# Kernel tuning notes

Hardware: AMD Instinct MI355X
Metric: run time of the kernel (lower is better)

The kernel has to match this reference:

```python
import jax, jax.numpy as jnp
import numpy as np

N_NODES = 100000

def _sage_conv(x, src, dst, deg_inv, Wl, bl, Wr):
    # PyG SAGEConv (aggr='mean', root_weight=True):
    #   out = lin_l(mean_{j in N(i)} x_j) + lin_r(x_i)
    msg = x[src]                                            # [E, d]
    agg = jax.ops.segment_sum(msg, dst, num_segments=N_NODES)  # [N, d]
    agg = agg * deg_inv                                     # mean (0 for isolated nodes)
    return agg @ Wl.T + bl + x @ Wr.T


def setup_inputs() -> dict:
    key = jax.random.key(0)
    ks = jax.random.split(key, 12)
    N, E, d_in, d_h, d_out = N_NODES, 1600000, 64, 64, 32
    x = jax.random.normal(ks[0], (N, d_in), dtype=jnp.float32)
    edge_index = jax.random.randint(ks[1], (2, E), 0, N, dtype=jnp.int64)

    def glorot(k, shape):
        fan_in = shape[1]
        return jax.random.normal(k, shape, dtype=jnp.float32) / np.sqrt(fan_in)

    return {
        "x": x,
        "edge_index": edge_index,
        "W1l": glorot(ks[2], (d_h, d_in)), "b1l": jnp.zeros((d_h,), jnp.float32), "W1r": glorot(ks[3], (d_h, d_in)),
        "W2l": glorot(ks[4], (d_h, d_h)),  "b2l": jnp.zeros((d_h,), jnp.float32), "W2r": glorot(ks[5], (d_h, d_h)),
        "W3l": glorot(ks[6], (d_h, d_h)),  "b3l": jnp.zeros((d_h,), jnp.float32), "W3r": glorot(ks[7], (d_h, d_h)),
        "Wfc": glorot(ks[8], (d_out, d_h)), "bfc": jnp.zeros((d_out,), jnp.float32),
    }


def reference(x, edge_index, W1l, b1l, W1r, W2l, b2l, W2r, W3l, b3l, W3r, Wfc, bfc):
    src, dst = edge_index[0], edge_index[1]
    # in-degree per destination node (shared by all three conv layers)
    ones = jnp.ones((src.shape[0],), x.dtype)
    deg = jax.ops.segment_sum(ones, dst, num_segments=N_NODES)
    deg_inv = (1.0 / jnp.maximum(deg, 1.0))[:, None]        # [N, 1]

    h = jax.nn.relu(_sage_conv(x, src, dst, deg_inv, W1l, b1l, W1r))
    # dropout(p=0.5) is identity in eval mode
    h = jax.nn.relu(_sage_conv(h, src, dst, deg_inv, W2l, b2l, W2r))
    h = jax.nn.relu(_sage_conv(h, src, dst, deg_inv, W3l, b3l, W3r))
    return h @ Wfc.T + bfc
```

## Files before the change

### kernel.cpp

```cpp
#include <hip/hip_runtime.h>
#include <hip/hip_fp16.h>

#define N_NODES 100000
#define D 64
#define BR 256
#define NB 391
#define ECH 4096
#define NROWPAD 100096

typedef _Float16 f16x8 __attribute__((ext_vector_type(8)));
typedef float f32x4 __attribute__((ext_vector_type(4)));

__device__ __forceinline__ float rlf(float v, int l) {
    union { float f; int i; } u;
    u.f = v;
    u.i = __builtin_amdgcn_readlane(u.i, l);
    return u.f;
}

__global__ __launch_bounds__(256) void k_cvt(const float4* __restrict__ x,
                                             uint2* __restrict__ y, int n4) {
    int i = blockIdx.x * 256 + threadIdx.x;
    if (i < n4) {
        float4 v = x[i];
        union { __half2 h[2]; uint2 u; } pk;
        pk.h[0] = __floats2half2_rn(v.x, v.y);
        pk.h[1] = __floats2half2_rn(v.z, v.w);
        y[i] = pk.u;
    }
}

__global__ __launch_bounds__(256) void k_prep(const float* __restrict__ Wl1, const float* __restrict__ Wr1,
                                              const float* __restrict__ Wl2, const float* __restrict__ Wr2,
                                              const float* __restrict__ Wl3, const float* __restrict__ Wr3,
                                              const float* __restrict__ Wfc,
                                              __half* __restrict__ Wf1, __half* __restrict__ Wf2,
                                              __half* __restrict__ Wf3, __half* __restrict__ Wffc,
                                              unsigned* __restrict__ x16, unsigned* __restrict__ H1,
                                              unsigned* __restrict__ H2) {
    int t = blockIdx.x * 256 + threadIdx.x;
    if (t < 24576) {
        int layer = t / 8192;
        int r = t % 8192;
        int f = r >> 9, rem = r & 511;
        int lane = rem >> 3, i = rem & 7;
        int kt = f >> 2, nt = f & 3;
        int k = kt * 32 + (lane >> 4) * 8 + i;
        int o = nt * 16 + (lane & 15);
        const float* Wl = layer == 0 ? Wl1 : layer == 1 ? Wl2 : Wl3;
        const float* Wr = layer == 0 ? Wr1 : layer == 1 ? Wr2 : Wr3;
        float v = (k < 64) ? Wl[o * 64 + k] : Wr[o * 64 + (k - 64)];
        __half* Wf = layer == 0 ? Wf1 : layer == 1 ? Wf2 : Wf3;
        Wf[r] = __float2half(v);
    } else if (t < 26624) {
        int r = t - 24576;
        int f = r >> 9, rem = r & 511;
        int lane = rem >> 3, i = rem & 7;
        int kt = f >> 1, nt = f & 1;
        int k = kt * 32 + (lane >> 4) * 8 + i;
        int o = nt * 16 + (lane & 15);
        Wffc[r] = __float2half(Wfc[o * 64 + k]);
    } else if (t < 26720) {
        int z = t - 26624;
        unsigned* buf = (z >> 5) == 0 ? x16 : (z >> 5) == 1 ? H1 : H2;
        buf[(size_t)N_NODES * 32 + (z & 31)] = 0u;
    }
}


__global__ __launch_bounds__(256) void k_hist(const int* __restrict__ dst,
                                              int* __restrict__ histT,
                                              int E, int ga) {
    __shared__ int h[NB];
    int blk = blockIdx.x, tid = threadIdx.x;
    for (int i = tid; i < NB; i += 256) h[i] = 0;
    __syncthreads();
    int base = blk * ECH;
    int lim = E - base; if (lim > ECH) lim = ECH;
    for (int i = tid; i < lim; i += 256)
        atomicAdd(&h[dst[base + i] >> 8], 1);
    __syncthreads();
    for (int i = tid; i < NB; i += 256)
        histT[i * ga + blk] = h[i];
}

__global__ __launch_bounds__(256) void k_scan1(const int* __restrict__ cnt,
                                               int* __restrict__ part,
                                               int* __restrict__ bsums) {
    __shared__ int s[256];
    int tid = threadIdx.x;
    int i4 = blockIdx.x * 256 + tid;
    int4 v = reinterpret_cast<const int4*>(cnt)[i4];
    int tsum = v.x + v.y + v.z + v.w;
    s[tid] = tsum;
    __syncthreads();
    for (int off = 1; off < 256; off <<= 1) {
        int t = 0;
        if (tid >= off) t = s[tid - off];
        __syncthreads();
        if (tid >= off) s[tid] += t;
        __syncthreads();
    }
    int excl = tid ? s[tid - 1] : 0;
    if (tid == 255) bsums[blockIdx.x] = s[255];
    int4 o;
    o.x = excl;
    o.y = o.x + v.x;
    o.z = o.y + v.y;
    o.w = o.z + v.z;
    reinterpret_cast<int4*>(part)[i4] = o;
}

__global__ __launch_bounds__(256) void k_scan2(int* __restrict__ bsums, int nb,
                                               int* __restrict__ col) {
    __shared__ int s[256];
    int tid = threadIdx.x;
    if (tid < 8) col[tid] = N_NODES;
    int v = (tid < nb) ? bsums[tid] : 0;
    s[tid] = v;
    __syncthreads();
    for (int off = 1; off < 256; off <<= 1) {
        int t = 0;
        if (tid >= off) t = s[tid - off];
        __syncthreads();
        if (tid >= off) s[tid] += t;
        __syncthreads();
    }
    if (tid < nb) bsums[tid] = tid ? s[tid - 1] : 0;
}

__global__ __launch_bounds__(256) void k_part(const int* __restrict__ src,
                                              const int* __restrict__ dst,
                                              const int* __restrict__ offs,
                                              const int* __restrict__ bsums,
                                              int* __restrict__ bedge,
                                              int E, int ga) {
    __shared__ int o[NB];
    int blk = blockIdx.x, tid = threadIdx.x;
    for (int i = tid; i < NB; i += 256) {
        int ent = i * ga + blk;
        o[i] = offs[ent] + bsums[ent >> 10];
    }
    __syncthreads();
    int base = blk * ECH;
    int lim = E - base; if (lim > ECH) lim = ECH;
    for (int i = tid; i < lim; i += 256) {
        int e = base + i;
        int d = dst[e];
        int pos = atomicAdd(&o[d >> 8], 1);
        bedge[pos] = src[e] | ((d & 255) << 17);
    }
}

__global__ __launch_bounds__(256) void k_csr(const int* __restrict__ bedge,
                                             const int* __restrict__ offs,
                                             const int* __restrict__ bsums,
                                             int* __restrict__ col,
                                             int2* __restrict__ rp,
                                             float* __restrict__ deg_inv,
                                             int E, int ga) {
    __shared__ int lcnt[BR];
    __shared__ int stmp[BR];
    __shared__ int lcur[BR];
    int b = blockIdx.x, tid = threadIdx.x;
    int e0 = b * ga;
    int ebeg = offs[e0] + bsums[e0 >> 10];
    int eend = E;
    if (b + 1 < NB) {
        int e1 = (b + 1) * ga;
        eend = offs[e1] + bsums[e1 >> 10];
    }
    int nbase = b * BR;
    int cbase = ebeg + b * (BR * 4) + 8;
    lcnt[tid] = 0;
    __syncthreads();
    for (int e = ebeg + tid; e < eend; e += 256)
        atomicAdd(&lcnt[bedge[e] >> 17], 1);
    __syncthreads();
    int v = lcnt[tid];
    int pdeg = (v + 3) & ~3;
    stmp[tid] = pdeg;
    __syncthreads();
    for (int off = 1; off < 256; off <<= 1) {
        int t = 0;
        if (tid >= off) t = stmp[tid - off];
        __syncthreads();
        if (tid >= off) stmp[tid] += t;
        __syncthreads();
    }
    int ex = tid ? stmp[tid - 1] : 0;
    int slot = cbase + ex;
    lcur[tid] = slot;
    int node = nbase + tid;
    if (node < N_NODES) {
        rp[node] = make_int2(slot, slot + pdeg);
        deg_inv[node] = 1.0f / (float)(v > 1 ? v : 1);
        for (int s2 = slot + v; s2 < slot + pdeg; ++s2) col[s2] = N_NODES;
    }
    __syncthreads();
    for (int e = ebeg + tid; e < eend; e += 256) {
        int ed = bedge[e];
        int pos = atomicAdd(&lcur[ed >> 17], 1);
        col[pos] = ed & 0x1FFFF;
    }
}


__global__ __launch_bounds__(256) void k_fused(const __half* __restrict__ Hin,
                                               __half* __restrict__ Hout,
                                               const __half* __restrict__ Wf,
                                               const float* __restrict__ bias,
                                               const int2* __restrict__ rp,
                                               const int* __restrict__ col,
                                               const float* __restrict__ deg_inv, int n) {
    __shared__ __half lds[4][16][72];
    int l = threadIdx.x & 63;
    int wv = threadIdx.x >> 6;
    int m0 = blockIdx.x * 64 + wv * 16;
    int q = l >> 4, li = l & 15;

    int beg = 0, nq = 0;
    float dinv = 0.f;
    if (l < 16 && m0 + l < n) {
        int2 se = rp[m0 + l];
        beg = se.x;
        nq = (se.y - se.x) >> 2;
        dinv = deg_inv[m0 + l];
    }
    const uint2* x8 = (const uint2*)Hin;
    const int* cq = col + q;

#pragma unroll
    for (int g = 0; g < 4; ++g) {
        int b0 = __builtin_amdgcn_readlane(beg, 4 * g + 0);
        int b1 = __builtin_amdgcn_readlane(beg, 4 * g + 1);
        int b2 = __builtin_amdgcn_readlane(beg, 4 * g + 2);
        int b3 = __builtin_amdgcn_readlane(beg, 4 * g + 3);
        int c0 = __builtin_amdgcn_readlane(nq, 4 * g + 0);
        int c1 = __builtin_amdgcn_readlane(nq, 4 * g + 1);
        int c2 = __builtin_amdgcn_readlane(nq, 4 * g + 2);
        int c3 = __builtin_amdgcn_readlane(nq, 4 * g + 3);
        int qmax = max(max(c0, c1), max(c2, c3));
        __half2 s00 = __floats2half2_rn(0.f, 0.f), s01 = s00;
        __half2 s10 = s00, s11 = s00, s20 = s00, s21 = s00, s30 = s00, s31 = s00;
        for (int qq = 0; qq < qmax; qq += 2) {
            int o = qq * 4;
            int a0 = qq < c0 ? b0 + o : 0;
            int a1 = qq < c1 ? b1 + o : 0;
            int a2 = qq < c2 ? b2 + o : 0;
            int a3 = qq < c3 ? b3 + o : 0;
            int a4 = qq + 1 < c0 ? b0 + o + 4 : 0;
            int a5 = qq + 1 < c1 ? b1 + o + 4 : 0;
            int a6 = qq + 1 < c2 ? b2 + o + 4 : 0;
            int a7 = qq + 1 < c3 ? b3 + o + 4 : 0;
            int i0 = cq[a0], i1 = cq[a1], i2 = cq[a2], i3 = cq[a3];
            int i4 = cq[a4], i5 = cq[a5], i6 = cq[a6], i7 = cq[a7];
            uint2 u0 = x8[(size_t)i0 * 16 + li];
            uint2 u1 = x8[(size_t)i1 * 16 + li];
            uint2 u2 = x8[(size_t)i2 * 16 + li];
            uint2 u3 = x8[(size_t)i3 * 16 + li];
            uint2 u4 = x8[(size_t)i4 * 16 + li];
            uint2 u5 = x8[(size_t)i5 * 16 + li];
            uint2 u6 = x8[(size_t)i6 * 16 + li];
            uint2 u7 = x8[(size_t)i7 * 16 + li];
            union { unsigned v; __half2 h; } w;
            w.v = u0.x; s00 = __hadd2(s00, w.h);
            w.v = u0.y; s01 = __hadd2(s01, w.h);
            w.v = u1.x; s10 = __hadd2(s10, w.h);
            w.v = u1.y; s11 = __hadd2(s11, w.h);
            w.v = u2.x; s20 = __hadd2(s20, w.h);
            w.v = u2.y; s21 = __hadd2(s21, w.h);
            w.v = u3.x; s30 = __hadd2(s30, w.h);
            w.v = u3.y; s31 = __hadd2(s31, w.h);
            w.v = u4.x; s00 = __hadd2(s00, w.h);
            w.v = u4.y; s01 = __hadd2(s01, w.h);
            w.v = u5.x; s10 = __hadd2(s10, w.h);
            w.v = u5.y; s11 = __hadd2(s11, w.h);
            w.v = u6.x; s20 = __hadd2(s20, w.h);
            w.v = u6.y; s21 = __hadd2(s21, w.h);
            w.v = u7.x; s30 = __hadd2(s30, w.h);
            w.v = u7.y; s31 = __hadd2(s31, w.h);
        }
        union { __half2 h; int i; } t;
#pragma unroll
        for (int m = 16; m < 64; m <<= 1) {
            t.h = s00; t.i = __shfl_xor(t.i, m); s00 = __hadd2(s00, t.h);
            t.h = s01; t.i = __shfl_xor(t.i, m); s01 = __hadd2(s01, t.h);
            t.h = s10; t.i = __shfl_xor(t.i, m); s10 = __hadd2(s10, t.h);
            t.h = s11; t.i = __shfl_xor(t.i, m); s11 = __hadd2(s11, t.h);
            t.h = s20; t.i = __shfl_xor(t.i, m); s20 = __hadd2(s20, t.h);
            t.h = s21; t.i = __shfl_xor(t.i, m); s21 = __hadd2(s21, t.h);
            t.h = s30; t.i = __shfl_xor(t.i, m); s30 = __hadd2(s30, t.h);
            t.h = s31; t.i = __shfl_xor(t.i, m); s31 = __hadd2(s31, t.h);
        }
        float d0 = rlf(dinv, 4 * g + 0);
        float d1 = rlf(dinv, 4 * g + 1);
        float d2 = rlf(dinv, 4 * g + 2);
        float d3 = rlf(dinv, 4 * g + 3);
        if (l < 16) {
            union { __half2 h; unsigned v; } p0, p1;
            float2 f;
            uint2 ov;
            f = __half22float2(s00); p0.h = __floats2half2_rn(f.x * d0, f.y * d0);
            f = __half22float2(s01); p1.h = __floats2half2_rn(f.x * d0, f.y * d0);
            ov.x = p0.v; ov.y = p1.v;
            *(uint2*)&lds[wv][4 * g + 0][li * 4] = ov;
            f = __half22float2(s10); p0.h = __floats2half2_rn(f.x * d1, f.y * d1);
            f = __half22float2(s11); p1.h = __floats2half2_rn(f.x * d1, f.y * d1);
            ov.x = p0.v; ov.y = p1.v;
            *(uint2*)&lds[wv][4 * g + 1][li * 4] = ov;
            f = __half22float2(s20); p0.h = __floats2half2_rn(f.x * d2, f.y * d2);
            f = __half22float2(s21); p1.h = __floats2half2_rn(f.x * d2, f.y * d2);
            ov.x = p0.v; ov.y = p1.v;
            *(uint2*)&lds[wv][4 * g + 2][li * 4] = ov;
            f = __half22float2(s30); p0.h = __floats2half2_rn(f.x * d3, f.y * d3);
            f = __half22float2(s31); p1.h = __floats2half2_rn(f.x * d3, f.y * d3);
            ov.x = p0.v; ov.y = p1.v;
            *(uint2*)&lds[wv][4 * g + 3][li * 4] = ov;
        }
    }

    const f16x8* wf8 = (const f16x8*)Wf;
    f16x8 bf[4][4];
#pragma unroll
    for (int kt = 0; kt < 4; ++kt)
#pragma unroll
        for (int nt = 0; nt < 4; ++nt)
            bf[kt][nt] = wf8[(kt * 4 + nt) * 64 + l];
    int rowA = li;
    f32x4 acc[4];
#pragma unroll
    for (int nt = 0; nt < 4; ++nt) {
        float bs = bias[nt * 16 + rowA];
        acc[nt] = (f32x4){bs, bs, bs, bs};
    }
#pragma unroll
    for (int kt = 0; kt < 4; ++kt) {
        f16x8 a;
        if (kt < 2)
            a = *(const f16x8*)&lds[wv][rowA][kt * 32 + q * 8];
        else
            a = *(const f16x8*)(Hin + (size_t)(m0 + rowA) * D + (kt - 2) * 32 + q * 8);
#pragma unroll
        for (int nt = 0; nt < 4; ++nt)
            acc[nt] = __builtin_amdgcn_mfma_f32_16x16x32_f16(a, bf[kt][nt], acc[nt], 0, 0, 0);
    }
#pragma unroll
    for (int nt = 0; nt < 4; ++nt)
#pragma unroll
        for (int qd = 0; qd < 4; ++qd) {
            int node = m0 + q * 4 + qd;
            float v = fmaxf(acc[nt][qd], 0.f);
            if (node < n)
                Hout[(size_t)node * D + nt * 16 + rowA] = __float2half(v);
        }
}


template <int KT, int NT, bool RELU, bool TWO, bool HOUT>
__global__ __launch_bounds__(256) void k_mgemm(const __half* __restrict__ A,
                                               const __half* __restrict__ X,
                                               const __half* __restrict__ Wf,
                                               const float* __restrict__ bias,
                                               void* __restrict__ outp, int n) {
    int l = threadIdx.x & 63;
    int wv = threadIdx.x >> 6;
    int m0 = blockIdx.x * 64 + wv * 16;
    int rowA = l & 15;
    int kg = l >> 4;
    const f16x8* wf8 = (const f16x8*)Wf;
    f16x8 b[KT][NT];
#pragma unroll
    for (int kt = 0; kt < KT; ++kt)
#pragma unroll
        for (int nt = 0; nt < NT; ++nt)
            b[kt][nt] = wf8[(kt * NT + nt) * 64 + l];
    f32x4 acc[NT];
#pragma unroll
    for (int nt = 0; nt < NT; ++nt) {
        float bs = bias[nt * 16 + rowA];
        acc[nt] = (f32x4){bs, bs, bs, bs};
    }
#pragma unroll
    for (int kt = 0; kt < KT; ++kt) {
        const __half* sp = (TWO && kt >= KT / 2) ? X : A;
        int ko = (TWO ? (kt & (KT / 2 - 1)) : kt) * 32;
        f16x8 a = *(const f16x8*)(sp + (size_t)(m0 + rowA) * D + ko + kg * 8);
#pragma unroll
        for (int nt = 0; nt < NT; ++nt)
            acc[nt] = __builtin_amdgcn_mfma_f32_16x16x32_f16(a, b[kt][nt], acc[nt], 0, 0, 0);
    }
#pragma unroll
    for (int nt = 0; nt < NT; ++nt)
#pragma unroll
        for (int q = 0; q < 4; ++q) {
            int node = m0 + kg * 4 + q;
            float v = acc[nt][q];
            if (RELU) v = fmaxf(v, 0.f);
            if (node < n) {
                if (HOUT)
                    ((__half*)outp)[(size_t)node * D + nt * 16 + rowA] = __float2half(v);
                else
                    ((float*)outp)[(size_t)node * (NT * 16) + nt * 16 + rowA] = v;
            }
        }
}


extern "C" void kernel_launch(void* const* d_in, const int* in_sizes, int n_in,
                              void* d_out, int out_size, void* d_ws, size_t ws_size,
                              hipStream_t stream) {
    const float* x   = (const float*)d_in[0];
    const int*   ei  = (const int*)d_in[1];
    const int    E   = in_sizes[1] / 2;
    const int*   src = ei;
    const int*   dst = ei + E;
    const float* W1l = (const float*)d_in[2];
    const float* b1l = (const float*)d_in[3];
    const float* W1r = (const float*)d_in[4];
    const float* W2l = (const float*)d_in[5];
    const float* b2l = (const float*)d_in[6];
    const float* W2r = (const float*)d_in[7];
    const float* W3l = (const float*)d_in[8];
    const float* b3l = (const float*)d_in[9];
    const float* W3r = (const float*)d_in[10];
    const float* Wfc = (const float*)d_in[11];
    const float* bfc = (const float*)d_in[12];
    float* out = (float*)d_out;

    const int ga      = (E + ECH - 1) / ECH;
    const int entries = NB * ga;
    const int padded  = (entries + 1023) & ~1023;
    const int nb2     = padded / 1024;

    char* p = (char*)d_ws;
    size_t off = 0;
    auto take = [&](size_t bytes) -> void* {
        void* r = p + off;
        off = (off + bytes + 255) & ~(size_t)255;
        return r;
    };
    __half* x16    = (__half*)take((size_t)NROWPAD * D * 2);
    __half* H1     = (__half*)take((size_t)NROWPAD * D * 2);
    __half* H2     = (__half*)take((size_t)NROWPAD * D * 2);
    float* deg_inv = (float*)take((size_t)N_NODES * 4);
    int2*  rp      = (int2*)take((size_t)N_NODES * 8);
    int*   histT   = (int*)take((size_t)padded * 4);
    int*   offs    = (int*)take((size_t)padded * 4);
    int*   bsums   = (int*)take(256 * 4);
    int*   bedge   = (int*)take((size_t)E * 4);
    int*   col     = (int*)take((size_t)(E + NB * BR * 4 + 72) * 4);
    __half* Wf1    = (__half*)take(8192 * 2);
    __half* Wf2    = (__half*)take(8192 * 2);
    __half* Wf3    = (__half*)take(8192 * 2);
    __half* Wffc   = (__half*)take(2048 * 2);

    k_prep<<<105, 256, 0, stream>>>(W1l, W1r, W2l, W2r, W3l, W3r, Wfc,
                                    Wf1, Wf2, Wf3, Wffc,
                                    (unsigned*)x16, (unsigned*)H1, (unsigned*)H2);
    int n4 = N_NODES * D / 4;
    k_cvt<<<(n4 + 255) / 256, 256, 0, stream>>>((const float4*)x, (uint2*)x16, n4);

    hipMemsetAsync(histT, 0, (size_t)padded * 4, stream);
    k_hist<<<ga, 256, 0, stream>>>(dst, histT, E, ga);
    k_scan1<<<nb2, 256, 0, stream>>>(histT, offs, bsums);
    k_scan2<<<1, 256, 0, stream>>>(bsums, nb2, col);
    k_part<<<ga, 256, 0, stream>>>(src, dst, offs, bsums, bedge, E, ga);
    k_csr<<<NB, 256, 0, stream>>>(bedge, offs, bsums, col, rp, deg_inv, E, ga);

    int gg = NROWPAD / 64;

    k_fused<<<gg, 256, 0, stream>>>(x16, H1, Wf1, b1l, rp, col, deg_inv, N_NODES);
    k_fused<<<gg, 256, 0, stream>>>(H1, H2, Wf2, b2l, rp, col, deg_inv, N_NODES);
    k_fused<<<gg, 256, 0, stream>>>(H2, H1, Wf3, b3l, rp, col, deg_inv, N_NODES);
    k_mgemm<2, 2, false, false, false><<<gg, 256, 0, stream>>>(H1, nullptr, Wffc, bfc, out, N_NODES);
}
```

Measured before the change: 187.4 us.

## Fuse final FC into third SAGE layer, fold memset into prep, retune partition

The final linear layer now runs inside the third fused SAGE kernel: the ReLU'd layer-3 tile is staged in LDS and multiplied by the FC weights. This removes a full write and re-read of H1 and one kernel launch. The histogram memset moves into the prep kernel, and the histogram and partition kernels use 512-thread blocks over smaller edge chunks for more parallelism. The trade-offs are more per-block histogram columns to scan and more LDS and register pressure in the last kernel.

```diff
diff --git a/kernel.cpp b/kernel.cpp
--- a/kernel.cpp
+++ b/kernel.cpp
@@ -5,7 +5,7 @@
 #define D 64
 #define BR 256
 #define NB 391
-#define ECH 4096
+#define ECH 2560
 #define NROWPAD 100096
 
 typedef _Float16 f16x8 __attribute__((ext_vector_type(8)));
@@ -37,7 +37,8 @@
                                               __half* __restrict__ Wf1, __half* __restrict__ Wf2,
                                               __half* __restrict__ Wf3, __half* __restrict__ Wffc,
                                               unsigned* __restrict__ x16, unsigned* __restrict__ H1,
-                                              unsigned* __restrict__ H2) {
+                                              unsigned* __restrict__ H2,
+                                              int* __restrict__ histT, int padded) {
     int t = blockIdx.x * 256 + threadIdx.x;
     if (t < 24576) {
         int layer = t / 8192;
@@ -64,23 +65,25 @@
         int z = t - 26624;
         unsigned* buf = (z >> 5) == 0 ? x16 : (z >> 5) == 1 ? H1 : H2;
         buf[(size_t)N_NODES * 32 + (z & 31)] = 0u;
-    }
-}
-
-
-__global__ __launch_bounds__(256) void k_hist(const int* __restrict__ dst,
+    } else if (t >= 32768 && t < 32768 + padded) {
+        histT[t - 32768] = 0;
+    }
+}
+
+
+__global__ __launch_bounds__(512) void k_hist(const int* __restrict__ dst,
                                               int* __restrict__ histT,
                                               int E, int ga) {
     __shared__ int h[NB];
     int blk = blockIdx.x, tid = threadIdx.x;
-    for (int i = tid; i < NB; i += 256) h[i] = 0;
+    for (int i = tid; i < NB; i += 512) h[i] = 0;
     __syncthreads();
     int base = blk * ECH;
     int lim = E - base; if (lim > ECH) lim = ECH;
-    for (int i = tid; i < lim; i += 256)
+    for (int i = tid; i < lim; i += 512)
         atomicAdd(&h[dst[base + i] >> 8], 1);
     __syncthreads();
-    for (int i = tid; i < NB; i += 256)
+    for (int i = tid; i < NB; i += 512)
         histT[i * ga + blk] = h[i];
 }
 
@@ -129,7 +132,7 @@
     if (tid < nb) bsums[tid] = tid ? s[tid - 1] : 0;
 }
 
-__global__ __launch_bounds__(256) void k_part(const int* __restrict__ src,
+__global__ __launch_bounds__(512) void k_part(const int* __restrict__ src,
                                               const int* __restrict__ dst,
                                               const int* __restrict__ offs,
                                               const int* __restrict__ bsums,
@@ -137,14 +140,14 @@
                                               int E, int ga) {
     __shared__ int o[NB];
     int blk = blockIdx.x, tid = threadIdx.x;
-    for (int i = tid; i < NB; i += 256) {
+    for (int i = tid; i < NB; i += 512) {
         int ent = i * ga + blk;
         o[i] = offs[ent] + bsums[ent >> 10];
     }
     __syncthreads();
     int base = blk * ECH;
     int lim = E - base; if (lim > ECH) lim = ECH;
-    for (int i = tid; i < lim; i += 256) {
+    for (int i = tid; i < lim; i += 512) {
         int e = base + i;
         int d = dst[e];
         int pos = atomicAdd(&o[d >> 8], 1);
@@ -206,19 +209,15 @@
 }
 
 
-__global__ __launch_bounds__(256) void k_fused(const __half* __restrict__ Hin,
-                                               __half* __restrict__ Hout,
-                                               const __half* __restrict__ Wf,
-                                               const float* __restrict__ bias,
-                                               const int2* __restrict__ rp,
-                                               const int* __restrict__ col,
-                                               const float* __restrict__ deg_inv, int n) {
-    __shared__ __half lds[4][16][72];
-    int l = threadIdx.x & 63;
-    int wv = threadIdx.x >> 6;
-    int m0 = blockIdx.x * 64 + wv * 16;
+__device__ __forceinline__ void fused_core(const __half* __restrict__ Hin,
+                                           const __half* __restrict__ Wf,
+                                           const float* __restrict__ bias,
+                                           const int2* __restrict__ rp,
+                                           const int* __restrict__ col,
+                                           const float* __restrict__ deg_inv, int n,
+                                           __half (&lds)[16][72], int m0, int l,
+                                           f32x4 (&acc)[4]) {
     int q = l >> 4, li = l & 15;
-
     int beg = 0, nq = 0;
     float dinv = 0.f;
     if (l < 16 && m0 + l < n) {
@@ -304,19 +303,19 @@
             f = __half22float2(s00); p0.h = __floats2half2_rn(f.x * d0, f.y * d0);
             f = __half22float2(s01); p1.h = __floats2half2_rn(f.x * d0, f.y * d0);
             ov.x = p0.v; ov.y = p1.v;
-            *(uint2*)&lds[wv][4 * g + 0][li * 4] = ov;
+            *(uint2*)&lds[4 * g + 0][li * 4] = ov;
             f = __half22float2(s10); p0.h = __floats2half2_rn(f.x * d1, f.y * d1);
             f = __half22float2(s11); p1.h = __floats2half2_rn(f.x * d1, f.y * d1);
             ov.x = p0.v; ov.y = p1.v;
-            *(uint2*)&lds[wv][4 * g + 1][li * 4] = ov;
+            *(uint2*)&lds[4 * g + 1][li * 4] = ov;
             f = __half22float2(s20); p0.h = __floats2half2_rn(f.x * d2, f.y * d2);
             f = __half22float2(s21); p1.h = __floats2half2_rn(f.x * d2, f.y * d2);
             ov.x = p0.v; ov.y = p1.v;
-            *(uint2*)&lds[wv][4 * g + 2][li * 4] = ov;
+            *(uint2*)&lds[4 * g + 2][li * 4] = ov;
             f = __half22float2(s30); p0.h = __floats2half2_rn(f.x * d3, f.y * d3);
             f = __half22float2(s31); p1.h = __floats2half2_rn(f.x * d3, f.y * d3);
             ov.x = p0.v; ov.y = p1.v;
-            *(uint2*)&lds[wv][4 * g + 3][li * 4] = ov;
+            *(uint2*)&lds[4 * g + 3][li * 4] = ov;
         }
     }
 
@@ -328,7 +327,6 @@
         for (int nt = 0; nt < 4; ++nt)
             bf[kt][nt] = wf8[(kt * 4 + nt) * 64 + l];
     int rowA = li;
-    f32x4 acc[4];
 #pragma unroll
     for (int nt = 0; nt < 4; ++nt) {
         float bs = bias[nt * 16 + rowA];
@@ -338,13 +336,29 @@
     for (int kt = 0; kt < 4; ++kt) {
         f16x8 a;
         if (kt < 2)
-            a = *(const f16x8*)&lds[wv][rowA][kt * 32 + q * 8];
+            a = *(const f16x8*)&lds[rowA][kt * 32 + q * 8];
         else
             a = *(const f16x8*)(Hin + (size_t)(m0 + rowA) * D + (kt - 2) * 32 + q * 8);
 #pragma unroll
         for (int nt = 0; nt < 4; ++nt)
             acc[nt] = __builtin_amdgcn_mfma_f32_16x16x32_f16(a, bf[kt][nt], acc[nt], 0, 0, 0);
     }
+}
+
+__global__ __launch_bounds__(256) void k_fused(const __half* __restrict__ Hin,
+                                               __half* __restrict__ Hout,
+                                               const __half* __restrict__ Wf,
+                                               const float* __restrict__ bias,
+                                               const int2* __restrict__ rp,
+                                               const int* __restrict__ col,
+                                               const float* __restrict__ deg_inv, int n) {
+    __shared__ __half lds[4][16][72];
+    int l = threadIdx.x & 63;
+    int wv = threadIdx.x >> 6;
+    int m0 = blockIdx.x * 64 + wv * 16;
+    f32x4 acc[4];
+    fused_core(Hin, Wf, bias, rp, col, deg_inv, n, lds[wv], m0, l, acc);
+    int q = l >> 4, rowA = l & 15;
 #pragma unroll
     for (int nt = 0; nt < 4; ++nt)
 #pragma unroll
@@ -356,53 +370,56 @@
         }
 }
 
-
-template <int KT, int NT, bool RELU, bool TWO, bool HOUT>
-__global__ __launch_bounds__(256) void k_mgemm(const __half* __restrict__ A,
-                                               const __half* __restrict__ X,
-                                               const __half* __restrict__ Wf,
-                                               const float* __restrict__ bias,
-                                               void* __restrict__ outp, int n) {
+__global__ __launch_bounds__(256) void k_fused_fc(const __half* __restrict__ Hin,
+                                                  float* __restrict__ out,
+                                                  const __half* __restrict__ Wf,
+                                                  const float* __restrict__ bias,
+                                                  const __half* __restrict__ Wffc,
+                                                  const float* __restrict__ bfc,
+                                                  const int2* __restrict__ rp,
+                                                  const int* __restrict__ col,
+                                                  const float* __restrict__ deg_inv, int n) {
+    __shared__ __half lds[4][16][72];
     int l = threadIdx.x & 63;
     int wv = threadIdx.x >> 6;
     int m0 = blockIdx.x * 64 + wv * 16;
-    int rowA = l & 15;
-    int kg = l >> 4;
-    const f16x8* wf8 = (const f16x8*)Wf;
-    f16x8 b[KT][NT];
-#pragma unroll
-    for (int kt = 0; kt < KT; ++kt)
-#pragma unroll
-        for (int nt = 0; nt < NT; ++nt)
-            b[kt][nt] = wf8[(kt * NT + nt) * 64 + l];
-    f32x4 acc[NT];
-#pragma unroll
-    for (int nt = 0; nt < NT; ++nt) {
-        float bs = bias[nt * 16 + rowA];
-        acc[nt] = (f32x4){bs, bs, bs, bs};
-    }
-#pragma unroll
-    for (int kt = 0; kt < KT; ++kt) {
-        const __half* sp = (TWO && kt >= KT / 2) ? X : A;
-        int ko = (TWO ? (kt & (KT / 2 - 1)) : kt) * 32;
-        f16x8 a = *(const f16x8*)(sp + (size_t)(m0 + rowA) * D + ko + kg * 8);
-#pragma unroll
-        for (int nt = 0; nt < NT; ++nt)
-            acc[nt] = __builtin_amdgcn_mfma_f32_16x16x32_f16(a, b[kt][nt], acc[nt], 0, 0, 0);
-    }
-#pragma unroll
-    for (int nt = 0; nt < NT; ++nt)
-#pragma unroll
-        for (int q = 0; q < 4; ++q) {
-            int node = m0 + kg * 4 + q;
-            float v = acc[nt][q];
-            if (RELU) v = fmaxf(v, 0.f);
-            if (node < n) {
-                if (HOUT)
-                    ((__half*)outp)[(size_t)node * D + nt * 16 + rowA] = __float2half(v);
-                else
-                    ((float*)outp)[(size_t)node * (NT * 16) + nt * 16 + rowA] = v;
-            }
+    f32x4 acc[4];
+    fused_core(Hin, Wf, bias, rp, col, deg_inv, n, lds[wv], m0, l, acc);
+    int q = l >> 4, li = l & 15;
+
+#pragma unroll
+    for (int nt = 0; nt < 4; ++nt)
+#pragma unroll
+        for (int qd = 0; qd < 4; ++qd)
+            lds[wv][q * 4 + qd][nt * 16 + li] = __float2half(fmaxf(acc[nt][qd], 0.f));
+
+    const f16x8* wfc8 = (const f16x8*)Wffc;
+    f16x8 bf2[2][2];
+#pragma unroll
+    for (int kt = 0; kt < 2; ++kt)
+#pragma unroll
+        for (int nt = 0; nt < 2; ++nt)
+            bf2[kt][nt] = wfc8[(kt * 2 + nt) * 64 + l];
+    f32x4 acc2[2];
+#pragma unroll
+    for (int nt = 0; nt < 2; ++nt) {
+        float bs = bfc[nt * 16 + li];
+        acc2[nt] = (f32x4){bs, bs, bs, bs};
+    }
+#pragma unroll
+    for (int kt = 0; kt < 2; ++kt) {
+        f16x8 a = *(const f16x8*)&lds[wv][li][kt * 32 + q * 8];
+#pragma unroll
+        for (int nt = 0; nt < 2; ++nt)
+            acc2[nt] = __builtin_amdgcn_mfma_f32_16x16x32_f16(a, bf2[kt][nt], acc2[nt], 0, 0, 0);
+    }
+#pragma unroll
+    for (int nt = 0; nt < 2; ++nt)
+#pragma unroll
+        for (int qd = 0; qd < 4; ++qd) {
+            int node = m0 + q * 4 + qd;
+            if (node < n)
+                out[(size_t)node * 32 + nt * 16 + li] = acc2[nt][qd];
         }
 }
 
@@ -455,23 +472,23 @@
     __half* Wf3    = (__half*)take(8192 * 2);
     __half* Wffc   = (__half*)take(2048 * 2);
 
-    k_prep<<<105, 256, 0, stream>>>(W1l, W1r, W2l, W2r, W3l, W3r, Wfc,
-                                    Wf1, Wf2, Wf3, Wffc,
-                                    (unsigned*)x16, (unsigned*)H1, (unsigned*)H2);
+    int gp = (32768 + padded + 255) / 256;
+    k_prep<<<gp, 256, 0, stream>>>(W1l, W1r, W2l, W2r, W3l, W3r, Wfc,
+                                   Wf1, Wf2, Wf3, Wffc,
+                                   (unsigned*)x16, (unsigned*)H1, (unsigned*)H2,
+                                   histT, padded);
     int n4 = N_NODES * D / 4;
     k_cvt<<<(n4 + 255) / 256, 256, 0, stream>>>((const float4*)x, (uint2*)x16, n4);
 
-    hipMemsetAsync(histT, 0, (size_t)padded * 4, stream);
-    k_hist<<<ga, 256, 0, stream>>>(dst, histT, E, ga);
+    k_hist<<<ga, 512, 0, stream>>>(dst, histT, E, ga);
     k_scan1<<<nb2, 256, 0, stream>>>(histT, offs, bsums);
     k_scan2<<<1, 256, 0, stream>>>(bsums, nb2, col);
-    k_part<<<ga, 256, 0, stream>>>(src, dst, offs, bsums, bedge, E, ga);
+    k_part<<<ga, 512, 0, stream>>>(src, dst, offs, bsums, bedge, E, ga);
     k_csr<<<NB, 256, 0, stream>>>(bedge, offs, bsums, col, rp, deg_inv, E, ga);
 
     int gg = NROWPAD / 64;
 
     k_fused<<<gg, 256, 0, stream>>>(x16, H1, Wf1, b1l, rp, col, deg_inv, N_NODES);
     k_fused<<<gg, 256, 0, stream>>>(H1, H2, Wf2, b2l, rp, col, deg_inv, N_NODES);
-    k_fused<<<gg, 256, 0, stream>>>(H2, H1, Wf3, b3l, rp, col, deg_inv, N_NODES);
-    k_mgemm<2, 2, false, false, false><<<gg, 256, 0, stream>>>(H1, nullptr, Wffc, bfc, out, N_NODES);
-}
+    k_fused_fc<<<gg, 256, 0, stream>>>(H2, out, Wf3, b3l, Wffc, bfc, rp, col, deg_inv, N_NODES);
+}
```

Measured after the change: 177.3 us. 5.4% less time.
